# Kernel tuning notes

Hardware: AMD Instinct MI355X
Metric: run time of the kernel (lower is better)

Reference implementation:

```python
import jax, jax.numpy as jnp
import numpy as np
from jax import lax

K = 3
EPS = 1e-5


def get_graph_feature(x, k):
    # Faithful to the torch code, including flat .view() reshapes (no transpose)
    B, N = x.shape[0], x.shape[1]          # num_points = x.size(1)
    x = x.reshape(B, -1, N)                # (B, C, N) flat reshape
    C = x.shape[1]
    inner = -2.0 * jnp.einsum('bcn,bcm->bnm', x, x)           # (B, N, N)
    xx = jnp.sum(x * x, axis=1, keepdims=True)                # (B, 1, N)
    dist = -xx - inner - jnp.swapaxes(xx, 1, 2)               # neg sq distances
    idx = lax.top_k(dist, k)[1]                               # (B, N, k) nearest
    flat = x.reshape(B * N, C)                                # flat reshape (as torch .view)
    idx_full = (idx + (jnp.arange(B) * N)[:, None, None]).reshape(-1)
    feature = flat[idx_full].reshape(B, N, k, C)
    xc = x.reshape(B, N, 1, C)                                # flat reshape (as torch .view)
    feature = jnp.concatenate([feature - xc, jnp.broadcast_to(xc, (B, N, k, C))], axis=3)
    return feature.reshape(B, 2 * C, k, N)                    # flat reshape (as torch .view)


def bn(h, g, b, m, v, axis):
    shape = [1] * h.ndim
    shape[axis] = -1
    inv = g.reshape(shape) / jnp.sqrt(v.reshape(shape) + EPS)
    return (h - m.reshape(shape)) * inv + b.reshape(shape)


def setup_inputs() -> dict:
    key = jax.random.key(0)
    ks = jax.random.split(key, 24)
    B, N = 8, 4096

    def bn_params(i, c):
        return {
            f'bn{i}_g': jax.random.uniform(ks[4 * (ord(i) % 4)], (c,), jnp.float32) + 0.5,
            f'bn{i}_b': jax.random.normal(jax.random.fold_in(key, 10 + ord(i)), (c,), jnp.float32) * 0.1,
            f'bn{i}_m': jax.random.normal(jax.random.fold_in(key, 20 + ord(i)), (c,), jnp.float32) * 0.1,
            f'bn{i}_v': jax.random.uniform(jax.random.fold_in(key, 30 + ord(i)), (c,), jnp.float32) + 0.5,
        }

    inp = {
        'x': jax.random.normal(ks[0], (B, N, 3), jnp.float32),
        'w1': jax.random.normal(ks[1], (64, 6), jnp.float32) * (1.0 / np.sqrt(6.0)),
        'wA': jax.random.normal(ks[2], (256, 82), jnp.float32) * (1.0 / np.sqrt(82.0)),
        'bA': jax.random.normal(ks[3], (256,), jnp.float32) * 0.01,
        'wB': jax.random.normal(ks[4], (128, 256), jnp.float32) * (1.0 / np.sqrt(256.0)),
        'bB': jax.random.normal(ks[5], (128,), jnp.float32) * 0.01,
        'wC': jax.random.normal(ks[6], (3, 128), jnp.float32) * (1.0 / np.sqrt(128.0)),
        'bC': jax.random.normal(ks[7], (3,), jnp.float32) * 0.01,
    }
    inp.update(bn_params('1', 64))
    inp.update(bn_params('A', 256))
    inp.update(bn_params('B', 128))
    return inp


def reference(x, w1, wA, bA, wB, bB, wC, bC,
              bn1_g, bn1_b, bn1_m, bn1_v,
              bnA_g, bnA_b, bnA_m, bnA_v,
              bnB_g, bnB_b, bnB_m, bnB_v):
    f = get_graph_feature(x, K)                         # (B, 6, K, N)
    h = jnp.einsum('oc,bckn->bokn', w1, f)              # 1x1 conv, no bias
    h = jax.nn.leaky_relu(bn(h, bn1_g, bn1_b, bn1_m, bn1_v, 1), 0.2)
    x1 = jnp.max(h, axis=-1)                            # (B, 64, K)  (max over N!)
    x2 = jnp.max(get_graph_feature(x1, K), axis=-1)     # (B, 6, K)   (conv2 unused in source)
    x3 = jnp.max(get_graph_feature(x2, K), axis=-1)     # (B, 6, K)
    x4 = jnp.max(get_graph_feature(x3, K), axis=-1)     # (B, 6, K)
    xc = jnp.concatenate([x1, x2, x3, x4], axis=1)      # (B, 82, K)
    p = jnp.max(xc, axis=-1)                            # adaptive_max_pool1d -> (B, 82)
    h = jax.nn.leaky_relu(bn(p @ wA.T + bA, bnA_g, bnA_b, bnA_m, bnA_v, 1), 0.2)
    h = jax.nn.leaky_relu(bn(h @ wB.T + bB, bnB_g, bnB_b, bnB_m, bnB_v, 1), 0.2)
    return jax.nn.softmax(h @ wC.T + bC, axis=1)        # (B, 3)
```

## Files before the change

### kernel.cpp

```cpp
#include <hip/hip_runtime.h>
#include <math.h>

#define NPTS 4096
#define EPSV 1e-5f

__global__ __launch_bounds__(256, 2) void k_knn1(const float* __restrict__ x,
                                                 int* __restrict__ idx1) {
  __shared__ float4 pts[NPTS + 8];
  __shared__ float cd[64][4][3];
  __shared__ int   ci[64][4][3];
  const int b   = blockIdx.x >> 6;
  const int blk = blockIdx.x & 63;
  const float* xb = x + b * (NPTS * 3);
  const int t = threadIdx.x;

  for (int m = t; m < NPTS; m += 256) {
    float a0 = xb[m], a1 = xb[NPTS + m], a2 = xb[2 * NPTS + m];
    float xx = a0 * a0; xx = fmaf(a1, a1, xx); xx = fmaf(a2, a2, xx);
    pts[m] = make_float4(a0, a1, a2, xx);
  }
  __syncthreads();

  const int p = t & 63;
  const int s = t >> 6;
  const int n = blk * 64 + p;
  const float4 pn = pts[n];
  const float p2x = 2.0f * pn.x, p2y = 2.0f * pn.y, p2z = 2.0f * pn.z;
  const float c0 = -pn.w;
  float d0 = -INFINITY, d1 = -INFINITY, d2 = -INFINITY;
  int   i0 = 0x7fffffff, i1 = 0x7fffffff, i2 = 0x7fffffff;
  const int mstart = s * 1024;
  const float4* __restrict__ pchunk = &pts[mstart];

  float4 qa[8];
#pragma unroll
  for (int j = 0; j < 8; ++j) qa[j] = pchunk[j];

  for (int mb = 0; mb < 1024; mb += 16) {
    float4 qb[8];
#pragma unroll
    for (int j = 0; j < 8; ++j) qb[j] = pchunk[mb + 8 + j];
#pragma unroll
    for (int j = 0; j < 8; ++j) {
      float4 q = qa[j];
      float d = fmaf(p2x, q.x, fmaf(p2y, q.y, fmaf(p2z, q.z, c0))) - q.w;
      if (d > d2) {
        int m = mstart + mb + j;
        if (d > d1) {
          bool g0 = d > d0;
          d2 = d1;            i2 = i1;
          d1 = g0 ? d0 : d;   i1 = g0 ? i0 : m;
          d0 = g0 ? d : d0;   i0 = g0 ? m : i0;
        } else {
          d2 = d; i2 = m;
        }
      }
    }
#pragma unroll
    for (int j = 0; j < 8; ++j) qa[j] = pchunk[mb + 16 + j];
#pragma unroll
    for (int j = 0; j < 8; ++j) {
      float4 q = qb[j];
      float d = fmaf(p2x, q.x, fmaf(p2y, q.y, fmaf(p2z, q.z, c0))) - q.w;
      if (d > d2) {
        int m = mstart + mb + 8 + j;
        if (d > d1) {
          bool g0 = d > d0;
          d2 = d1;            i2 = i1;
          d1 = g0 ? d0 : d;   i1 = g0 ? i0 : m;
          d0 = g0 ? d : d0;   i0 = g0 ? m : i0;
        } else {
          d2 = d; i2 = m;
        }
      }
    }
  }

  cd[p][s][0] = d0; cd[p][s][1] = d1; cd[p][s][2] = d2;
  ci[p][s][0] = i0; ci[p][s][1] = i1; ci[p][s][2] = i2;
  __syncthreads();

  if (t < 64) {
    int* op = idx1 + (b * NPTS + blk * 64 + t) * 3;
    float pd = INFINITY; int pi = -1;
    for (int r = 0; r < 3; ++r) {
      float bd = -INFINITY; int bi = 0x7fffffff;
      for (int sc = 0; sc < 4; ++sc) {
        for (int kk = 0; kk < 3; ++kk) {
          float dv = cd[t][sc][kk]; int iv = ci[t][sc][kk];
          bool allowed = (dv < pd) || (dv == pd && iv > pi);
          bool better  = (dv > bd) || (dv == bd && iv < bi);
          if (allowed && better) { bd = dv; bi = iv; }
        }
      }
      op[r] = bi;
      pd = bd; pi = bi;
    }
  }
}

__global__ __launch_bounds__(256) void k_convmax(const float* __restrict__ x,
                                                 const int* __restrict__ idx1,
                                                 const float* __restrict__ w1,
                                                 float* __restrict__ pmax) {
  __shared__ float4 Ft4[128][2];
  __shared__ float  w1s[384];
  __shared__ float  smax[4][64];
  const int b    = blockIdx.x / 96;
  const int rr   = blockIdx.x - b * 96;
  const int kk   = rr >> 5;
  const int tile = rr & 31;
  const int t = threadIdx.x;
  for (int i = t; i < 384; i += 256) w1s[i] = w1[i];
  const float* xb = x + b * 12288;
  const int*   ib = idx1 + b * 12288;

  const int tn = t & 127, ch = t >> 7;
  const int n = tile * 128 + tn;
  float* ftrow = (float*)&Ft4[tn][0];
#pragma unroll
  for (int j = 0; j < 3; ++j) {
    int c = ch * 3 + j;
    int ofs = c * 12288 + kk * 4096 + n;
    int np  = ofs / 18;
    int rem = ofs - np * 18;
    int kp  = rem / 6;
    int cp  = rem - kp * 6;
    float val;
    if (cp < 3) {
      int jj = ib[np * 3 + kp];
      val = xb[jj * 3 + cp] - xb[np * 3 + cp];
    } else {
      val = xb[np * 3 + cp - 3];
    }
    ftrow[c] = val;
  }
  __syncthreads();

  const int o = t & 63, sub = t >> 6;
  float w[6];
#pragma unroll
  for (int c = 0; c < 6; ++c) w[c] = w1s[o * 6 + c];
  const int base = sub * 32;
  float mx = -INFINITY;

  float4 ra[4][2];
#pragma unroll
  for (int r = 0; r < 4; ++r) { ra[r][0] = Ft4[base + r][0]; ra[r][1] = Ft4[base + r][1]; }

  for (int i = 0; i < 32; i += 8) {
    float4 rb[4][2];
#pragma unroll
    for (int r = 0; r < 4; ++r) {
      rb[r][0] = Ft4[base + i + 4 + r][0];
      rb[r][1] = Ft4[base + i + 4 + r][1];
    }
#pragma unroll
    for (int r = 0; r < 4; ++r) {
      float h = w[0] * ra[r][0].x;
      h = fmaf(w[1], ra[r][0].y, h);
      h = fmaf(w[2], ra[r][0].z, h);
      h = fmaf(w[3], ra[r][0].w, h);
      h = fmaf(w[4], ra[r][1].x, h);
      h = fmaf(w[5], ra[r][1].y, h);
      mx = fmaxf(mx, h);
    }
#pragma unroll
    for (int r = 0; r < 4; ++r) {
      int nr = base + ((i + 8 + r) & 31);
      ra[r][0] = Ft4[nr][0]; ra[r][1] = Ft4[nr][1];
    }
#pragma unroll
    for (int r = 0; r < 4; ++r) {
      float h = w[0] * rb[r][0].x;
      h = fmaf(w[1], rb[r][0].y, h);
      h = fmaf(w[2], rb[r][0].z, h);
      h = fmaf(w[3], rb[r][0].w, h);
      h = fmaf(w[4], rb[r][1].x, h);
      h = fmaf(w[5], rb[r][1].y, h);
      mx = fmaxf(mx, h);
    }
  }
  smax[sub][o] = mx;
  __syncthreads();
  if (t < 64) {
    float m01 = fmaxf(smax[0][t], smax[1][t]);
    float m23 = fmaxf(smax[2][t], smax[3][t]);
    pmax[((b * 3 + kk) * 64 + t) * 32 + tile] = fmaxf(m01, m23);
  }
}

__device__ __forceinline__ void top3_insert(float d, int m,
                                            float& d0, float& d1, float& d2,
                                            int& i0, int& i1, int& i2) {
  if (d > d2) {
    bool g1 = d > d1;
    bool g0 = d > d0;
    d2 = g1 ? d1 : d;                 i2 = g1 ? i1 : m;
    d1 = g0 ? d0 : (g1 ? d : d1);     i1 = g0 ? i0 : (g1 ? m : i1);
    d0 = g0 ? d : d0;                 i0 = g0 ? m : i0;
  }
}

__global__ __launch_bounds__(256) void k_tail(
    const float* __restrict__ pmax,
    const float* __restrict__ bn1g, const float* __restrict__ bn1b,
    const float* __restrict__ bn1m, const float* __restrict__ bn1v,
    const float* __restrict__ wA, const float* __restrict__ bA,
    const float* __restrict__ bnAg, const float* __restrict__ bnAb,
    const float* __restrict__ bnAm, const float* __restrict__ bnAv,
    const float* __restrict__ wB, const float* __restrict__ bB,
    const float* __restrict__ bnBg, const float* __restrict__ bnBb,
    const float* __restrict__ bnBm, const float* __restrict__ bnBv,
    const float* __restrict__ wC, const float* __restrict__ bC,
    float* __restrict__ out) {
  __shared__ float a1[192];
  __shared__ int   idx2[192];
  __shared__ float a2[18], a3[18], a4[18];
  __shared__ int   idxs[18];
  __shared__ float pv[82];
  __shared__ float hA[256];
  __shared__ float hB[128];
  __shared__ float lg[3];
  const int b = blockIdx.x;
  const int t = threadIdx.x;

  if (t < 192) {
    int o = t / 3, k = t - o * 3;
    const float4* p4 = (const float4*)(pmax + ((b * 3 + k) * 64 + o) * 32);
    float4 v[8];
#pragma unroll
    for (int j = 0; j < 8; ++j) v[j] = p4[j];
    float mx = -INFINITY;
#pragma unroll
    for (int j = 0; j < 8; ++j) {
      mx = fmaxf(mx, fmaxf(fmaxf(v[j].x, v[j].y), fmaxf(v[j].z, v[j].w)));
    }
    float inv = bn1g[o] / sqrtf(bn1v[o] + EPSV);
    float val = (mx - bn1m[o]) * inv + bn1b[o];
    a1[o * 3 + k] = val >= 0.f ? val : 0.2f * val;
  }
  __syncthreads();

  if (t < 64) {
    float px = a1[t], py = a1[64 + t], pz = a1[128 + t];
    float pp = px * px; pp = fmaf(py, py, pp); pp = fmaf(pz, pz, pp);
    float d0 = -INFINITY, d1 = -INFINITY, d2 = -INFINITY;
    int i0 = 0, i1 = 0, i2 = 0;
#pragma unroll 8
    for (int m = 0; m < 64; ++m) {
      float qx = a1[m], qy = a1[64 + m], qz = a1[128 + m];
      float qq = qx * qx; qq = fmaf(qy, qy, qq); qq = fmaf(qz, qz, qq);
      float dot = px * qx; dot = fmaf(py, qy, dot); dot = fmaf(pz, qz, dot);
      float d = 2.f * dot - pp - qq;
      top3_insert(d, m, d0, d1, d2, i0, i1, i2);
    }
    idx2[t * 3 + 0] = i0; idx2[t * 3 + 1] = i1; idx2[t * 3 + 2] = i2;
  }
  __syncthreads();

  if (t < 18) {
    int o = t / 3, kk = t - o * 3;
    float mx = -INFINITY;
#pragma unroll 8
    for (int nn = 0; nn < 64; ++nn) {
      int ofs = o * 192 + kk * 64 + nn;
      int np = ofs / 18; int rem = ofs - np * 18;
      int kp = rem / 6;  int cp  = rem - kp * 6;
      float val = (cp < 3) ? (a1[idx2[np * 3 + kp] * 3 + cp] - a1[np * 3 + cp])
                           : a1[np * 3 + cp - 3];
      mx = fmaxf(mx, val);
    }
    a2[t] = mx;
  }
  __syncthreads();

  for (int stage = 0; stage < 2; ++stage) {
    const float* src = (stage == 0) ? a2 : a3;
    float*       dst = (stage == 0) ? a3 : a4;
    if (t < 6) {
      float px = src[t], py = src[6 + t], pz = src[12 + t];
      float pp = px * px; pp = fmaf(py, py, pp); pp = fmaf(pz, pz, pp);
      float d0 = -INFINITY, d1 = -INFINITY, d2 = -INFINITY;
      int i0 = 0, i1 = 0, i2 = 0;
#pragma unroll
      for (int m = 0; m < 6; ++m) {
        float qx = src[m], qy = src[6 + m], qz = src[12 + m];
        float qq = qx * qx; qq = fmaf(qy, qy, qq); qq = fmaf(qz, qz, qq);
        float dot = px * qx; dot = fmaf(py, qy, dot); dot = fmaf(pz, qz, dot);
        float d = 2.f * dot - pp - qq;
        top3_insert(d, m, d0, d1, d2, i0, i1, i2);
      }
      idxs[t * 3 + 0] = i0; idxs[t * 3 + 1] = i1; idxs[t * 3 + 2] = i2;
    }
    __syncthreads();
    if (t < 18) {
      int o = t / 3, kk = t - o * 3;
      float mx = -INFINITY;
#pragma unroll
      for (int nn = 0; nn < 6; ++nn) {
        int ofs = o * 18 + kk * 6 + nn;
        int np = ofs / 18; int rem = ofs - np * 18;
        int kp = rem / 6;  int cp  = rem - kp * 6;
        float val = (cp < 3) ? (src[idxs[np * 3 + kp] * 3 + cp] - src[np * 3 + cp])
                             : src[np * 3 + cp - 3];
        mx = fmaxf(mx, val);
      }
      dst[t] = mx;
    }
    __syncthreads();
  }

  if (t < 82) {
    float mx;
    if (t < 64)      { int o = t;      mx = fmaxf(fmaxf(a1[o*3], a1[o*3+1]), a1[o*3+2]); }
    else if (t < 70) { int o = t - 64; mx = fmaxf(fmaxf(a2[o*3], a2[o*3+1]), a2[o*3+2]); }
    else if (t < 76) { int o = t - 70; mx = fmaxf(fmaxf(a3[o*3], a3[o*3+1]), a3[o*3+2]); }
    else             { int o = t - 76; mx = fmaxf(fmaxf(a4[o*3], a4[o*3+1]), a4[o*3+2]); }
    pv[t] = mx;
  }
  __syncthreads();

  {
    float acc = bA[t];
    const float* wr = wA + t * 82;
#pragma unroll 8
    for (int i = 0; i < 82; ++i) acc = fmaf(wr[i], pv[i], acc);
    float inv = bnAg[t] / sqrtf(bnAv[t] + EPSV);
    float v = (acc - bnAm[t]) * inv + bnAb[t];
    hA[t] = v >= 0.f ? v : 0.2f * v;
  }
  __syncthreads();

  if (t < 128) {
    float acc = bB[t];
    const float4* wr4 = (const float4*)(wB + t * 256);
#pragma unroll 8
    for (int i = 0; i < 64; ++i) {
      float4 wv = wr4[i];
      acc = fmaf(wv.x, hA[4 * i + 0], acc);
      acc = fmaf(wv.y, hA[4 * i + 1], acc);
      acc = fmaf(wv.z, hA[4 * i + 2], acc);
      acc = fmaf(wv.w, hA[4 * i + 3], acc);
    }
    float inv = bnBg[t] / sqrtf(bnBv[t] + EPSV);
    float v = (acc - bnBm[t]) * inv + bnBb[t];
    hB[t] = v >= 0.f ? v : 0.2f * v;
  }
  __syncthreads();

  if (t < 3) {
    float acc = bC[t];
    const float* wr = wC + t * 128;
#pragma unroll 8
    for (int i = 0; i < 128; ++i) acc = fmaf(wr[i], hB[i], acc);
    lg[t] = acc;
  }
  __syncthreads();
  if (t == 0) {
    float m = fmaxf(fmaxf(lg[0], lg[1]), lg[2]);
    float e0 = expf(lg[0] - m), e1 = expf(lg[1] - m), e2 = expf(lg[2] - m);
    float s = e0 + e1 + e2;
    out[b * 3 + 0] = e0 / s;
    out[b * 3 + 1] = e1 / s;
    out[b * 3 + 2] = e2 / s;
  }
}

extern "C" void kernel_launch(void* const* d_in, const int* in_sizes, int n_in,
                              void* d_out, int out_size, void* d_ws, size_t ws_size,
                              hipStream_t stream) {
  (void)in_sizes; (void)n_in; (void)out_size; (void)ws_size;
  const float* x    = (const float*)d_in[0];
  const float* w1   = (const float*)d_in[1];
  const float* wA   = (const float*)d_in[2];
  const float* bA   = (const float*)d_in[3];
  const float* wB   = (const float*)d_in[4];
  const float* bB   = (const float*)d_in[5];
  const float* wC   = (const float*)d_in[6];
  const float* bC   = (const float*)d_in[7];
  const float* bn1g = (const float*)d_in[8];
  const float* bn1b = (const float*)d_in[9];
  const float* bn1m = (const float*)d_in[10];
  const float* bn1v = (const float*)d_in[11];
  const float* bnAg = (const float*)d_in[12];
  const float* bnAb = (const float*)d_in[13];
  const float* bnAm = (const float*)d_in[14];
  const float* bnAv = (const float*)d_in[15];
  const float* bnBg = (const float*)d_in[16];
  const float* bnBb = (const float*)d_in[17];
  const float* bnBm = (const float*)d_in[18];
  const float* bnBv = (const float*)d_in[19];
  float* out = (float*)d_out;

  int*   idx1 = (int*)d_ws;
  float* pmax = (float*)((char*)d_ws + 8 * 4096 * 3 * 4);

  k_knn1<<<512, 256, 0, stream>>>(x, idx1);
  k_convmax<<<768, 256, 0, stream>>>(x, idx1, w1, pmax);
  k_tail<<<8, 256, 0, stream>>>(pmax,
                                bn1g, bn1b, bn1m, bn1v,
                                wA, bA, bnAg, bnAb, bnAm, bnAv,
                                wB, bB, bnBg, bnBb, bnBm, bnBv,
                                wC, bC, out);
}
```

Before: 192.1 us.

## Replace per-point top-3 insertion with two-pass threshold filtering in kNN kernel

The kNN kernel now makes two passes over the point set. The first pass computes only per-slice maxima using packed two-wide float math on structure-of-arrays shared memory. The top three of the eight slice maxima give a lower-bound threshold, and a second pass collects every candidate at or above it through shared atomics, capped at 24. A final exact top-3 runs over those candidates. This removes the branchy insertion logic and doubles the threads per block, at the cost of computing distances twice and risking overflow of the candidate buffer when many points tie.

After: 182.7 us. -4.9%, faster.

```diff
diff --git a/kernel.cpp b/kernel.cpp
--- a/kernel.cpp
+++ b/kernel.cpp
@@ -4,94 +4,131 @@
 #define NPTS 4096
 #define EPSV 1e-5f
 
-__global__ __launch_bounds__(256, 2) void k_knn1(const float* __restrict__ x,
+typedef float v2f __attribute__((ext_vector_type(2)));
+
+__device__ __forceinline__ v2f max2(v2f a, v2f b) {
+  v2f r; r.x = fmaxf(a.x, b.x); r.y = fmaxf(a.y, b.y); return r;
+}
+
+__device__ __forceinline__ v2f key2(v2f qx, v2f qy, v2f qz, v2f nw,
+                                    v2f p2x, v2f p2y, v2f p2z) {
+  return p2x * qx + (p2y * qy + (p2z * qz + nw));
+}
+
+__global__ __launch_bounds__(512, 4) void k_knn1(const float* __restrict__ x,
                                                  int* __restrict__ idx1) {
-  __shared__ float4 pts[NPTS + 8];
-  __shared__ float cd[64][4][3];
-  __shared__ int   ci[64][4][3];
+  __shared__ float qxs[NPTS + 8], qys[NPTS + 8], qzs[NPTS + 8], qws[NPTS + 8];
+  __shared__ float scmax[64][8];
+  __shared__ float theta[64];
+  __shared__ int   ccnt[64];
+  __shared__ int   cands[64][24];
   const int b   = blockIdx.x >> 6;
   const int blk = blockIdx.x & 63;
   const float* xb = x + b * (NPTS * 3);
   const int t = threadIdx.x;
 
-  for (int m = t; m < NPTS; m += 256) {
+  for (int m = t; m < NPTS; m += 512) {
     float a0 = xb[m], a1 = xb[NPTS + m], a2 = xb[2 * NPTS + m];
-    float xx = a0 * a0; xx = fmaf(a1, a1, xx); xx = fmaf(a2, a2, xx);
-    pts[m] = make_float4(a0, a1, a2, xx);
+    float w = a0 * a0; w = fmaf(a1, a1, w); w = fmaf(a2, a2, w);
+    qxs[m] = a0; qys[m] = a1; qzs[m] = a2; qws[m] = -w;
+  }
+  if (t < 64) ccnt[t] = 0;
+  if (t >= 504) {
+    int m = NPTS + (t - 504);
+    qxs[m] = 0.f; qys[m] = 0.f; qzs[m] = 0.f; qws[m] = -INFINITY;
   }
   __syncthreads();
 
   const int p = t & 63;
   const int s = t >> 6;
   const int n = blk * 64 + p;
-  const float4 pn = pts[n];
-  const float p2x = 2.0f * pn.x, p2y = 2.0f * pn.y, p2z = 2.0f * pn.z;
-  const float c0 = -pn.w;
-  float d0 = -INFINITY, d1 = -INFINITY, d2 = -INFINITY;
-  int   i0 = 0x7fffffff, i1 = 0x7fffffff, i2 = 0x7fffffff;
-  const int mstart = s * 1024;
-  const float4* __restrict__ pchunk = &pts[mstart];
-
-  float4 qa[8];
-#pragma unroll
-  for (int j = 0; j < 8; ++j) qa[j] = pchunk[j];
-
-  for (int mb = 0; mb < 1024; mb += 16) {
-    float4 qb[8];
-#pragma unroll
-    for (int j = 0; j < 8; ++j) qb[j] = pchunk[mb + 8 + j];
-#pragma unroll
-    for (int j = 0; j < 8; ++j) {
-      float4 q = qa[j];
-      float d = fmaf(p2x, q.x, fmaf(p2y, q.y, fmaf(p2z, q.z, c0))) - q.w;
-      if (d > d2) {
-        int m = mstart + mb + j;
-        if (d > d1) {
-          bool g0 = d > d0;
-          d2 = d1;            i2 = i1;
-          d1 = g0 ? d0 : d;   i1 = g0 ? i0 : m;
-          d0 = g0 ? d : d0;   i0 = g0 ? m : i0;
-        } else {
-          d2 = d; i2 = m;
+  const float pxv = qxs[n], pyv = qys[n], pzv = qzs[n];
+  const v2f p2x = {2.f * pxv, 2.f * pxv};
+  const v2f p2y = {2.f * pyv, 2.f * pyv};
+  const v2f p2z = {2.f * pzv, 2.f * pzv};
+  const int m0 = s * 512;
+  const float* bx = &qxs[m0]; const float* by = &qys[m0];
+  const float* bz = &qzs[m0]; const float* bw = &qws[m0];
+
+  v2f vm = {-INFINITY, -INFINITY};
+  float4 ax0 = *(const float4*)&bx[0], ax1 = *(const float4*)&bx[4];
+  float4 ay0 = *(const float4*)&by[0], ay1 = *(const float4*)&by[4];
+  float4 az0 = *(const float4*)&bz[0], az1 = *(const float4*)&bz[4];
+  float4 aw0 = *(const float4*)&bw[0], aw1 = *(const float4*)&bw[4];
+  for (int j = 0; j < 512; j += 8) {
+    float4 nx0 = *(const float4*)&bx[j + 8], nx1 = *(const float4*)&bx[j + 12];
+    float4 ny0 = *(const float4*)&by[j + 8], ny1 = *(const float4*)&by[j + 12];
+    float4 nz0 = *(const float4*)&bz[j + 8], nz1 = *(const float4*)&bz[j + 12];
+    float4 nw0 = *(const float4*)&bw[j + 8], nw1 = *(const float4*)&bw[j + 12];
+    v2f k0 = key2((v2f){ax0.x, ax0.y}, (v2f){ay0.x, ay0.y}, (v2f){az0.x, az0.y}, (v2f){aw0.x, aw0.y}, p2x, p2y, p2z);
+    v2f k1 = key2((v2f){ax0.z, ax0.w}, (v2f){ay0.z, ay0.w}, (v2f){az0.z, az0.w}, (v2f){aw0.z, aw0.w}, p2x, p2y, p2z);
+    v2f k2 = key2((v2f){ax1.x, ax1.y}, (v2f){ay1.x, ay1.y}, (v2f){az1.x, az1.y}, (v2f){aw1.x, aw1.y}, p2x, p2y, p2z);
+    v2f k3 = key2((v2f){ax1.z, ax1.w}, (v2f){ay1.z, ay1.w}, (v2f){az1.z, az1.w}, (v2f){aw1.z, aw1.w}, p2x, p2y, p2z);
+    vm = max2(vm, max2(max2(k0, k1), max2(k2, k3)));
+    ax0 = nx0; ax1 = nx1; ay0 = ny0; ay1 = ny1;
+    az0 = nz0; az1 = nz1; aw0 = nw0; aw1 = nw1;
+  }
+  scmax[p][s] = fmaxf(vm.x, vm.y);
+  __syncthreads();
+
+  if (t < 64) {
+    float d0 = -INFINITY, d1 = -INFINITY, d2 = -INFINITY;
+#pragma unroll
+    for (int ss = 0; ss < 8; ++ss) {
+      float v = scmax[t][ss];
+      float nd2 = fmaxf(d2, fminf(d1, v));
+      float nd1 = fmaxf(d1, fminf(d0, v));
+      d0 = fmaxf(d0, v); d1 = nd1; d2 = nd2;
+    }
+    theta[t] = d2;
+  }
+  __syncthreads();
+  const float th = theta[p];
+
+  ax0 = *(const float4*)&bx[0]; ax1 = *(const float4*)&bx[4];
+  ay0 = *(const float4*)&by[0]; ay1 = *(const float4*)&by[4];
+  az0 = *(const float4*)&bz[0]; az1 = *(const float4*)&bz[4];
+  aw0 = *(const float4*)&bw[0]; aw1 = *(const float4*)&bw[4];
+  for (int j = 0; j < 512; j += 8) {
+    float4 nx0 = *(const float4*)&bx[j + 8], nx1 = *(const float4*)&bx[j + 12];
+    float4 ny0 = *(const float4*)&by[j + 8], ny1 = *(const float4*)&by[j + 12];
+    float4 nz0 = *(const float4*)&bz[j + 8], nz1 = *(const float4*)&bz[j + 12];
+    float4 nw0 = *(const float4*)&bw[j + 8], nw1 = *(const float4*)&bw[j + 12];
+    v2f k0 = key2((v2f){ax0.x, ax0.y}, (v2f){ay0.x, ay0.y}, (v2f){az0.x, az0.y}, (v2f){aw0.x, aw0.y}, p2x, p2y, p2z);
+    v2f k1 = key2((v2f){ax0.z, ax0.w}, (v2f){ay0.z, ay0.w}, (v2f){az0.z, az0.w}, (v2f){aw0.z, aw0.w}, p2x, p2y, p2z);
+    v2f k2 = key2((v2f){ax1.x, ax1.y}, (v2f){ay1.x, ay1.y}, (v2f){az1.x, az1.y}, (v2f){aw1.x, aw1.y}, p2x, p2y, p2z);
+    v2f k3 = key2((v2f){ax1.z, ax1.w}, (v2f){ay1.z, ay1.w}, (v2f){az1.z, az1.w}, (v2f){aw1.z, aw1.w}, p2x, p2y, p2z);
+    v2f mc = max2(max2(k0, k1), max2(k2, k3));
+    float mm = fmaxf(mc.x, mc.y);
+    if (mm >= th) {
+      float kk[8] = {k0.x, k0.y, k1.x, k1.y, k2.x, k2.y, k3.x, k3.y};
+#pragma unroll
+      for (int u = 0; u < 8; ++u) {
+        if (kk[u] >= th) {
+          int c = atomicAdd(&ccnt[p], 1);
+          if (c < 24) cands[p][c] = m0 + j + u;
         }
       }
     }
-#pragma unroll
-    for (int j = 0; j < 8; ++j) qa[j] = pchunk[mb + 16 + j];
-#pragma unroll
-    for (int j = 0; j < 8; ++j) {
-      float4 q = qb[j];
-      float d = fmaf(p2x, q.x, fmaf(p2y, q.y, fmaf(p2z, q.z, c0))) - q.w;
-      if (d > d2) {
-        int m = mstart + mb + 8 + j;
-        if (d > d1) {
-          bool g0 = d > d0;
-          d2 = d1;            i2 = i1;
-          d1 = g0 ? d0 : d;   i1 = g0 ? i0 : m;
-          d0 = g0 ? d : d0;   i0 = g0 ? m : i0;
-        } else {
-          d2 = d; i2 = m;
-        }
-      }
-    }
-  }
-
-  cd[p][s][0] = d0; cd[p][s][1] = d1; cd[p][s][2] = d2;
-  ci[p][s][0] = i0; ci[p][s][1] = i1; ci[p][s][2] = i2;
+    ax0 = nx0; ax1 = nx1; ay0 = ny0; ay1 = ny1;
+    az0 = nz0; az1 = nz1; aw0 = nw0; aw1 = nw1;
+  }
   __syncthreads();
 
   if (t < 64) {
-    int* op = idx1 + (b * NPTS + blk * 64 + t) * 3;
+    int cnt = ccnt[t]; if (cnt > 24) cnt = 24;
+    const int nn = blk * 64 + t;
+    const float P2X = 2.f * qxs[nn], P2Y = 2.f * qys[nn], P2Z = 2.f * qzs[nn];
+    int* op = idx1 + (b * NPTS + nn) * 3;
     float pd = INFINITY; int pi = -1;
     for (int r = 0; r < 3; ++r) {
       float bd = -INFINITY; int bi = 0x7fffffff;
-      for (int sc = 0; sc < 4; ++sc) {
-        for (int kk = 0; kk < 3; ++kk) {
-          float dv = cd[t][sc][kk]; int iv = ci[t][sc][kk];
-          bool allowed = (dv < pd) || (dv == pd && iv > pi);
-          bool better  = (dv > bd) || (dv == bd && iv < bi);
-          if (allowed && better) { bd = dv; bi = iv; }
-        }
+      for (int c = 0; c < cnt; ++c) {
+        int m = cands[t][c];
+        float kv = fmaf(P2X, qxs[m], fmaf(P2Y, qys[m], fmaf(P2Z, qzs[m], qws[m])));
+        bool allowed = (kv < pd) || (kv == pd && m > pi);
+        bool better  = (kv > bd) || (kv == bd && m < bi);
+        if (allowed && better) { bd = kv; bi = m; }
       }
       op[r] = bi;
       pd = bd; pi = bi;
@@ -396,7 +433,7 @@
   int*   idx1 = (int*)d_ws;
   float* pmax = (float*)((char*)d_ws + 8 * 4096 * 3 * 4);
 
-  k_knn1<<<512, 256, 0, stream>>>(x, idx1);
+  k_knn1<<<512, 512, 0, stream>>>(x, idx1);
   k_convmax<<<768, 256, 0, stream>>>(x, idx1, w1, pmax);
   k_tail<<<8, 256, 0, stream>>>(pmax,
                                 bn1g, bn1b, bn1m, bn1v,
```

## Prepack points into float4 global buffer and read kNN candidates from global

Applied to the files above, without the earlier changes.

A new pack kernel writes each point as (x,y,z,-|x|^2) into a workspace buffer. The kNN kernel drops its shared-memory staging of all 4096 points and its manual double-buffering, and instead streams candidates straight from global memory through cache with wave-uniform addressing. This removes the per-block shared-memory fill and the large LDS footprint, which should allow more occupancy, and it folds the norm into one fma. In exchange it adds a kernel launch, relies on L1/L2 for reuse, and the qpack buffer aliases pmax, which is only safe because convmax overwrites pmax after knn1 has finished.

Result: slower. 241.8 us (+25.9%).

```diff
diff --git a/kernel.cpp b/kernel.cpp
--- a/kernel.cpp
+++ b/kernel.cpp
@@ -4,74 +4,49 @@
 #define NPTS 4096
 #define EPSV 1e-5f
 
-__global__ __launch_bounds__(256, 2) void k_knn1(const float* __restrict__ x,
-                                                 int* __restrict__ idx1) {
-  __shared__ float4 pts[NPTS + 8];
+__global__ __launch_bounds__(256) void k_pack(const float* __restrict__ x,
+                                              float4* __restrict__ qpack) {
+  const int i = blockIdx.x * 256 + threadIdx.x;
+  const int b = i >> 12, m = i & 4095;
+  const float* xb = x + b * 12288;
+  float a0 = xb[m], a1 = xb[NPTS + m], a2 = xb[2 * NPTS + m];
+  float w = -fmaf(a2, a2, fmaf(a1, a1, a0 * a0));
+  qpack[i] = make_float4(a0, a1, a2, w);
+}
+
+__global__ __launch_bounds__(256) void k_knn1(const float4* __restrict__ qpack,
+                                              int* __restrict__ idx1) {
   __shared__ float cd[64][4][3];
   __shared__ int   ci[64][4][3];
-  const int b   = blockIdx.x >> 6;
-  const int blk = blockIdx.x & 63;
-  const float* xb = x + b * (NPTS * 3);
+  const int b     = blockIdx.x >> 6;
+  const int pr    = blockIdx.x & 63;
+  const int pbase = pr * 64;
   const int t = threadIdx.x;
-
-  for (int m = t; m < NPTS; m += 256) {
-    float a0 = xb[m], a1 = xb[NPTS + m], a2 = xb[2 * NPTS + m];
-    float xx = a0 * a0; xx = fmaf(a1, a1, xx); xx = fmaf(a2, a2, xx);
-    pts[m] = make_float4(a0, a1, a2, xx);
-  }
-  __syncthreads();
-
   const int p = t & 63;
-  const int s = t >> 6;
-  const int n = blk * 64 + p;
-  const float4 pn = pts[n];
-  const float p2x = 2.0f * pn.x, p2y = 2.0f * pn.y, p2z = 2.0f * pn.z;
-  const float c0 = -pn.w;
+  const int s = __builtin_amdgcn_readfirstlane(t >> 6);
+
+  const float4 pv = qpack[b * NPTS + pbase + p];
+  const float p2x = 2.f * pv.x, p2y = 2.f * pv.y, p2z = 2.f * pv.z;
+
+  const float4* __restrict__ qp = qpack + b * NPTS + s * 1024;
+
   float d0 = -INFINITY, d1 = -INFINITY, d2 = -INFINITY;
   int   i0 = 0x7fffffff, i1 = 0x7fffffff, i2 = 0x7fffffff;
   const int mstart = s * 1024;
-  const float4* __restrict__ pchunk = &pts[mstart];
-
-  float4 qa[8];
-#pragma unroll
-  for (int j = 0; j < 8; ++j) qa[j] = pchunk[j];
-
-  for (int mb = 0; mb < 1024; mb += 16) {
-    float4 qb[8];
-#pragma unroll
-    for (int j = 0; j < 8; ++j) qb[j] = pchunk[mb + 8 + j];
-#pragma unroll
-    for (int j = 0; j < 8; ++j) {
-      float4 q = qa[j];
-      float d = fmaf(p2x, q.x, fmaf(p2y, q.y, fmaf(p2z, q.z, c0))) - q.w;
-      if (d > d2) {
-        int m = mstart + mb + j;
-        if (d > d1) {
-          bool g0 = d > d0;
-          d2 = d1;            i2 = i1;
-          d1 = g0 ? d0 : d;   i1 = g0 ? i0 : m;
-          d0 = g0 ? d : d0;   i0 = g0 ? m : i0;
-        } else {
-          d2 = d; i2 = m;
-        }
-      }
-    }
-#pragma unroll
-    for (int j = 0; j < 8; ++j) qa[j] = pchunk[mb + 16 + j];
-#pragma unroll
-    for (int j = 0; j < 8; ++j) {
-      float4 q = qb[j];
-      float d = fmaf(p2x, q.x, fmaf(p2y, q.y, fmaf(p2z, q.z, c0))) - q.w;
-      if (d > d2) {
-        int m = mstart + mb + 8 + j;
-        if (d > d1) {
-          bool g0 = d > d0;
-          d2 = d1;            i2 = i1;
-          d1 = g0 ? d0 : d;   i1 = g0 ? i0 : m;
-          d0 = g0 ? d : d0;   i0 = g0 ? m : i0;
-        } else {
-          d2 = d; i2 = m;
-        }
+
+#pragma unroll 8
+  for (int j = 0; j < 1024; ++j) {
+    float4 q = qp[j];
+    float d = fmaf(p2x, q.x, fmaf(p2y, q.y, fmaf(p2z, q.z, q.w)));
+    if (d > d2) {
+      int m = mstart + j;
+      if (d > d1) {
+        bool g0 = d > d0;
+        d2 = d1;            i2 = i1;
+        d1 = g0 ? d0 : d;   i1 = g0 ? i0 : m;
+        d0 = g0 ? d : d0;   i0 = g0 ? m : i0;
+      } else {
+        d2 = d; i2 = m;
       }
     }
   }
@@ -81,7 +56,7 @@
   __syncthreads();
 
   if (t < 64) {
-    int* op = idx1 + (b * NPTS + blk * 64 + t) * 3;
+    int* op = idx1 + (b * NPTS + pbase + t) * 3;
     float pd = INFINITY; int pi = -1;
     for (int r = 0; r < 3; ++r) {
       float bd = -INFINITY; int bi = 0x7fffffff;
@@ -393,10 +368,12 @@
   const float* bnBv = (const float*)d_in[19];
   float* out = (float*)d_out;
 
-  int*   idx1 = (int*)d_ws;
-  float* pmax = (float*)((char*)d_ws + 8 * 4096 * 3 * 4);
-
-  k_knn1<<<512, 256, 0, stream>>>(x, idx1);
+  int*    idx1  = (int*)d_ws;
+  float4* qpack = (float4*)((char*)d_ws + 8 * 4096 * 3 * 4);
+  float*  pmax  = (float*)((char*)d_ws + 8 * 4096 * 3 * 4);
+
+  k_pack<<<128, 256, 0, stream>>>(x, qpack);
+  k_knn1<<<512, 256, 0, stream>>>(qpack, idx1);
   k_convmax<<<768, 256, 0, stream>>>(x, idx1, w1, pmax);
   k_tail<<<8, 256, 0, stream>>>(pmax,
                                 bn1g, bn1b, bn1m, bn1v,
```
